# Performance work log

Measured on AMD Instinct MI355X. Metric: run time of the kernel, lower is better.

## Reference

```python
import jax, jax.numpy as jnp
import numpy as np

# Static config (matches init_kwargs / input_specs)
B, CIN, H, W = 8, 32, 96, 96
OC, KH, KW = 64, 3, 3
SH, SW = 1, 1
PAD = 1
P = 3                      # num_points
POS_MIN, POS_MAX = -1.0, 1.0
OH = (H + 2 * PAD - KH) // SH + 1   # 96
OW = (W + 2 * PAD - KW) // SW + 1   # 96
K = CIN * KH * KW                    # 288 reduction elements
S = OH * OW                          # 9216 output positions


def setup_inputs() -> dict:
    key = jax.random.key(0)
    k1, k2, k3 = jax.random.split(key, 3)
    x = jax.random.normal(k1, (B, CIN, H, W), dtype=jnp.float32)
    # positions: shared linspace over position_range, expanded per weight
    pos = jnp.broadcast_to(
        jnp.linspace(POS_MIN, POS_MAX, P, dtype=jnp.float32),
        (OC, CIN, KH, KW, P),
    )
    # values: linear ramp between two small random endpoints (start, end)
    start = 0.01 * jax.random.normal(k2, (OC, CIN, KH, KW), dtype=jnp.float32)
    end = 0.01 * jax.random.normal(k3, (OC, CIN, KH, KW), dtype=jnp.float32)
    w = jnp.linspace(0.0, 1.0, P, dtype=jnp.float32)
    values = start[..., None] * (1.0 - w) + end[..., None] * w
    return {"x": x, "positions": pos, "values": values}


def _unfold(x):
    """F.unfold equivalent: [B,CIN,H,W] -> [B, CIN*KH*KW, OH*OW], (c,kh,kw) order."""
    xp = jnp.pad(x, ((0, 0), (0, 0), (PAD, PAD), (PAD, PAD)))
    cols = [
        xp[:, :, kh : kh + OH * SH : SH, kw : kw + OW * SW : SW]
        for kh in range(KH)
        for kw in range(KW)
    ]
    patches = jnp.stack(cols, axis=2)  # [B, CIN, KH*KW, OH, OW]
    return patches.reshape(B, K, S)


def _piecewise_conv(x, positions, values):
    patches = _unfold(x)                      # [B, K, S]
    pos = positions.reshape(OC, K, P)
    val = values.reshape(OC, K, P)
    dp = pos[..., 1:] - pos[..., :-1]         # [OC, K, P-1]
    dv = val[..., 1:] - val[..., :-1]
    # slope 0 on degenerate intervals (pos_i == pos_{i+1} contributes val_i, as in kernel)
    slopes = jnp.where(dp > 0, dv / jnp.where(dp > 0, dp, 1.0), 0.0)

    # f(x) = val_0 + sum_i slope_i * (clip(x, pos_i, pos_{i+1}) - pos_i)
    # Exactly reproduces the kernel's piecewise-linear interp with left/right clamping
    # for sorted positions. Scan over the K reduction axis keeps the [B,OC,S]
    # broadcast intermediate small.
    xs = (
        patches.transpose(1, 0, 2),   # [K, B, S]
        pos.transpose(1, 0, 2),       # [K, OC, P]
        val.transpose(1, 0, 2),       # [K, OC, P]
        slopes.transpose(1, 0, 2),    # [K, OC, P-1]
    )

    def step(acc, inp):
        xk, pk, vk, sk = inp          # [B,S], [OC,P], [OC,P], [OC,P-1]
        f = jnp.broadcast_to(vk[None, :, 0, None], (B, OC, S))
        for i in range(P - 1):        # P is small & static
            t = jnp.clip(xk[:, None, :], pk[None, :, i, None], pk[None, :, i + 1, None])
            f = f + sk[None, :, i, None] * (t - pk[None, :, i, None])
        return acc + f, None

    out, _ = jax.lax.scan(step, jnp.zeros((B, OC, S), x.dtype), xs)
    return out.reshape(B, OC, OH, OW)


def reference(x, positions, values):
    return _piecewise_conv(x, positions, values)
```

## Files before the change

### kernel.cpp

```cpp
#include <hip/hip_runtime.h>


typedef _Float16 half8 __attribute__((ext_vector_type(8)));
typedef float floatx4 __attribute__((ext_vector_type(4)));
typedef float floatx16 __attribute__((ext_vector_type(16)));

#define CIN   32
#define OCN   64
#define HW    96
#define NCOL  98
#define NSTEP 36
#define WS_A_HALVES (NSTEP * 2 * 64 * 8)

__global__ __launch_bounds__(128) void prep_kernel(
    const float* __restrict__ pos, const float* __restrict__ val,
    _Float16* __restrict__ wsA, float* __restrict__ bias) {
  const int oc = blockIdx.x;
  const int t = threadIdx.x;
  __shared__ float csum[128];
  float cacc = 0.f;
  const float p0 = pos[0], p1 = pos[1], p2 = pos[2];
  const float r01 = (p1 > p0) ? 1.f / (p1 - p0) : 0.f;
  const float r12 = (p2 > p1) ? 1.f / (p2 - p1) : 0.f;
  if (t < 72) {
    const int s = t >> 1, khalf = t & 1;
    const int kk = s >> 1, s2 = s & 1;
    const int khkw = kk >> 1, c2 = kk & 1;
    half8 h;
#pragma unroll
    for (int j = 0; j < 8; ++j) {
      const int cin = s2 * 16 + khalf * 8 + j;
      const float* vb = val + ((size_t)(oc * CIN + cin) * 9 + khkw) * 3;
      const float V0 = vb[0], V1 = vb[1], V2 = vb[2];
      const float s0 = (V1 - V0) * r01, s1 = (V2 - V1) * r12;
      h[j] = (_Float16)(c2 ? s1 : s0);
      if (c2 == 0) cacc += V0 - s0 * p0 - s1 * p1;
    }
    *reinterpret_cast<half8*>(
        &wsA[(((size_t)s * 2 + (oc >> 5)) * 64 + khalf * 32 + (oc & 31)) * 8]) = h;
  }
  csum[t] = cacc;
  __syncthreads();
  for (int st = 64; st > 0; st >>= 1) {
    if (t < st) csum[t] += csum[t + st];
    __syncthreads();
  }
  if (t == 0) bias[oc] = csum[0];
}

__global__ __launch_bounds__(384, 5) void pwconv_kernel(
    const float* __restrict__ x, const float* __restrict__ pos,
    const _Float16* __restrict__ wsA, const float* __restrict__ bias,
    float* __restrict__ out) {
  const int blk = blockIdx.x;
  const int b  = blk & 7;
  const int oh = blk >> 3;
  const int tid = threadIdx.x;

  __shared__ alignas(16) _Float16 Bs[2 * 3 * 4 * NCOL * 8];

  const float p0 = pos[0], p1 = pos[1], p2 = pos[2];

  const int lane = tid & 63;
  const int wv   = tid >> 6;
  const int mG   = wv >> 1 == 0 ? 0 : (wv >= 3 ? 1 : 0);
  const int mG2  = wv / 3;
  const int nf   = wv % 3;
  const int l31  = lane & 31;
  const int q2   = lane >> 5;
  (void)mG;

  const _Float16* abase = wsA + (size_t)lane * 8;
  half8 a_cur = *reinterpret_cast<const half8*>(abase + (size_t)(0 * 2 + mG2) * 64 * 8);

  if (tid < 288) {
    const int cg  = tid % 24;
    const int t2  = tid / 24;
    const int chi = t2 & 3;
    const int row = t2 >> 2;
    const int xr = oh + row - 1;
    floatx4 v[8];
    if (xr >= 0 && xr < HW) {
      const float* src = x + (((size_t)b * CIN + chi * 8) * HW + xr) * HW + cg * 4;
#pragma unroll
      for (int j = 0; j < 8; ++j)
        v[j] = *reinterpret_cast<const floatx4*>(src + (size_t)j * HW * HW);
    } else {
#pragma unroll
      for (int j = 0; j < 8; ++j) v[j] = (floatx4){0.f, 0.f, 0.f, 0.f};
    }
#pragma unroll
    for (int c = 0; c < 4; ++c) {
      half8 a0, a1;
#pragma unroll
      for (int j = 0; j < 8; ++j) {
        const float tv = v[j][c];
        a0[j] = (_Float16)fminf(fmaxf(tv, p0), p1);
        a1[j] = (_Float16)fminf(fmaxf(tv, p1), p2);
      }
      const int col = 1 + cg * 4 + c;
      *reinterpret_cast<half8*>(&Bs[(((0 * 3 + row) * 4 + chi) * NCOL + col) * 8]) = a0;
      *reinterpret_cast<half8*>(&Bs[(((1 * 3 + row) * 4 + chi) * NCOL + col) * 8]) = a1;
    }
  } else if (tid < 312) {
    const int ht = tid - 288;
    const int col = (ht & 1) ? 97 : 0;
    const int chi = (ht >> 1) & 3;
    const int row = ht >> 3;
    const _Float16 h0 = (_Float16)fminf(fmaxf(0.f, p0), p1);
    const _Float16 h1 = (_Float16)fminf(fmaxf(0.f, p1), p2);
    half8 a0, a1;
#pragma unroll
    for (int j = 0; j < 8; ++j) { a0[j] = h0; a1[j] = h1; }
    *reinterpret_cast<half8*>(&Bs[(((0 * 3 + row) * 4 + chi) * NCOL + col) * 8]) = a0;
    *reinterpret_cast<half8*>(&Bs[(((1 * 3 + row) * 4 + chi) * NCOL + col) * 8]) = a1;
  }
  __syncthreads();

  floatx16 acc;
#pragma unroll
  for (int i = 0; i < 16; ++i) acc[i] = 0.f;

  const int lbase = q2 * NCOL + nf * 32 + l31;

#pragma unroll
  for (int s = 0; s < NSTEP; ++s) {
    half8 a_nxt;
    if (s + 1 < NSTEP)
      a_nxt = *reinterpret_cast<const half8*>(
          abase + (size_t)((s + 1) * 2 + mG2) * 64 * 8);
    const int khkw = s >> 2;
    const int c2   = (s >> 1) & 1;
    const int s2   = s & 1;
    const int kh   = khkw / 3;
    const int kw   = khkw - kh * 3;
    const half8 bf = *reinterpret_cast<const half8*>(
        &Bs[(((c2 * 3 + kh) * 4 + s2 * 2) * NCOL + kw + lbase) * 8]);
    acc = __builtin_amdgcn_mfma_f32_32x32x16_f16(a_cur, bf, acc, 0, 0, 0);
    a_cur = a_nxt;
  }

  const int ow = nf * 32 + l31;
#pragma unroll
  for (int g = 0; g < 4; ++g) {
    const int ocb = mG2 * 32 + g * 8 + q2 * 4;
    const floatx4 bv = *reinterpret_cast<const floatx4*>(&bias[ocb]);
#pragma unroll
    for (int i = 0; i < 4; ++i) {
      const size_t idx = (((size_t)b * OCN + ocb + i) * HW + oh) * HW + ow;
      out[idx] = acc[g * 4 + i] + bv[i];
    }
  }
}

extern "C" void kernel_launch(void* const* d_in, const int* in_sizes, int n_in,
                              void* d_out, int out_size, void* d_ws, size_t ws_size,
                              hipStream_t stream) {
  const float* x   = (const float*)d_in[0];
  const float* pos = (const float*)d_in[1];
  const float* val = (const float*)d_in[2];
  _Float16* wsA = (_Float16*)d_ws;
  float* bias = (float*)((char*)d_ws + WS_A_HALVES * 2);
  float* outp = (float*)d_out;

  prep_kernel<<<64, 128, 0, stream>>>(pos, val, wsA, bias);
  pwconv_kernel<<<8 * HW, 384, 0, stream>>>(x, pos, wsA, bias, outp);
}
```

Before: 79.61 us.

## Split K across waves with per-wave 3 N-tiles and LDS reduction

Changes the work split from 6 waves each owning one 32x32 output tile over the full K=36 steps to 4 waves, each owning an OC half and a K half (c2) across all three N tiles. Each A fragment is reused across three MFMAs, so global A loads per MFMA drop, and the two K halves are summed through LDS before the store. This adds an extra barrier and an LDS reduction, uses more accumulator registers, and lowers the thread count per block.

```diff
diff --git a/kernel.cpp b/kernel.cpp
--- a/kernel.cpp
+++ b/kernel.cpp
@@ -9,8 +9,7 @@
 #define OCN   64
 #define HW    96
 #define NCOL  98
-#define NSTEP 36
-#define WS_A_HALVES (NSTEP * 2 * 64 * 8)
+#define WS_A_HALVES (36 * 2 * 64 * 8)
 
 __global__ __launch_bounds__(128) void prep_kernel(
     const float* __restrict__ pos, const float* __restrict__ val,
@@ -48,7 +47,7 @@
   if (t == 0) bias[oc] = csum[0];
 }
 
-__global__ __launch_bounds__(384, 5) void pwconv_kernel(
+__global__ __launch_bounds__(256, 3) void pwconv_kernel(
     const float* __restrict__ x, const float* __restrict__ pos,
     const _Float16* __restrict__ wsA, const float* __restrict__ bias,
     float* __restrict__ out) {
@@ -63,92 +62,118 @@
 
   const int lane = tid & 63;
   const int wv   = tid >> 6;
-  const int mG   = wv >> 1 == 0 ? 0 : (wv >= 3 ? 1 : 0);
-  const int mG2  = wv / 3;
-  const int nf   = wv % 3;
+  const int mG2  = wv & 1;
+  const int c2   = wv >> 1;
   const int l31  = lane & 31;
   const int q2   = lane >> 5;
-  (void)mG;
 
   const _Float16* abase = wsA + (size_t)lane * 8;
-  half8 a_cur = *reinterpret_cast<const half8*>(abase + (size_t)(0 * 2 + mG2) * 64 * 8);
+#define AGIDX(s) ((size_t)((((s) >> 1) * 4 + c2 * 2 + ((s) & 1)) * 2 + mG2) * 64 * 8)
+  half8 a0 = *reinterpret_cast<const half8*>(abase + AGIDX(0));
+  half8 a1 = *reinterpret_cast<const half8*>(abase + AGIDX(1));
 
-  if (tid < 288) {
-    const int cg  = tid % 24;
-    const int t2  = tid / 24;
-    const int chi = t2 & 3;
-    const int row = t2 >> 2;
-    const int xr = oh + row - 1;
-    floatx4 v[8];
-    if (xr >= 0 && xr < HW) {
-      const float* src = x + (((size_t)b * CIN + chi * 8) * HW + xr) * HW + cg * 4;
+  for (int it = tid; it < 312; it += 256) {
+    if (it < 288) {
+      const int cg  = it % 24;
+      const int t2  = it / 24;
+      const int chi = t2 & 3;
+      const int row = t2 >> 2;
+      const int xr = oh + row - 1;
+      floatx4 v[8];
+      if (xr >= 0 && xr < HW) {
+        const float* src = x + (((size_t)b * CIN + chi * 8) * HW + xr) * HW + cg * 4;
 #pragma unroll
-      for (int j = 0; j < 8; ++j)
-        v[j] = *reinterpret_cast<const floatx4*>(src + (size_t)j * HW * HW);
+        for (int j = 0; j < 8; ++j)
+          v[j] = *reinterpret_cast<const floatx4*>(src + (size_t)j * HW * HW);
+      } else {
+#pragma unroll
+        for (int j = 0; j < 8; ++j) v[j] = (floatx4){0.f, 0.f, 0.f, 0.f};
+      }
+#pragma unroll
+      for (int c = 0; c < 4; ++c) {
+        half8 h0, h1;
+#pragma unroll
+        for (int j = 0; j < 8; ++j) {
+          const float tv = v[j][c];
+          h0[j] = (_Float16)fminf(fmaxf(tv, p0), p1);
+          h1[j] = (_Float16)fminf(fmaxf(tv, p1), p2);
+        }
+        const int col = 1 + cg * 4 + c;
+        *reinterpret_cast<half8*>(&Bs[(((0 * 3 + row) * 4 + chi) * NCOL + col) * 8]) = h0;
+        *reinterpret_cast<half8*>(&Bs[(((1 * 3 + row) * 4 + chi) * NCOL + col) * 8]) = h1;
+      }
     } else {
+      const int ht = it - 288;
+      const int col = (ht & 1) ? 97 : 0;
+      const int chi = (ht >> 1) & 3;
+      const int row = ht >> 3;
+      const _Float16 z0 = (_Float16)fminf(fmaxf(0.f, p0), p1);
+      const _Float16 z1 = (_Float16)fminf(fmaxf(0.f, p1), p2);
+      half8 h0, h1;
 #pragma unroll
-      for (int j = 0; j < 8; ++j) v[j] = (floatx4){0.f, 0.f, 0.f, 0.f};
+      for (int j = 0; j < 8; ++j) { h0[j] = z0; h1[j] = z1; }
+      *reinterpret_cast<half8*>(&Bs[(((0 * 3 + row) * 4 + chi) * NCOL + col) * 8]) = h0;
+      *reinterpret_cast<half8*>(&Bs[(((1 * 3 + row) * 4 + chi) * NCOL + col) * 8]) = h1;
     }
-#pragma unroll
-    for (int c = 0; c < 4; ++c) {
-      half8 a0, a1;
-#pragma unroll
-      for (int j = 0; j < 8; ++j) {
-        const float tv = v[j][c];
-        a0[j] = (_Float16)fminf(fmaxf(tv, p0), p1);
-        a1[j] = (_Float16)fminf(fmaxf(tv, p1), p2);
-      }
-      const int col = 1 + cg * 4 + c;
-      *reinterpret_cast<half8*>(&Bs[(((0 * 3 + row) * 4 + chi) * NCOL + col) * 8]) = a0;
-      *reinterpret_cast<half8*>(&Bs[(((1 * 3 + row) * 4 + chi) * NCOL + col) * 8]) = a1;
-    }
-  } else if (tid < 312) {
-    const int ht = tid - 288;
-    const int col = (ht & 1) ? 97 : 0;
-    const int chi = (ht >> 1) & 3;
-    const int row = ht >> 3;
-    const _Float16 h0 = (_Float16)fminf(fmaxf(0.f, p0), p1);
-    const _Float16 h1 = (_Float16)fminf(fmaxf(0.f, p1), p2);
-    half8 a0, a1;
-#pragma unroll
-    for (int j = 0; j < 8; ++j) { a0[j] = h0; a1[j] = h1; }
-    *reinterpret_cast<half8*>(&Bs[(((0 * 3 + row) * 4 + chi) * NCOL + col) * 8]) = a0;
-    *reinterpret_cast<half8*>(&Bs[(((1 * 3 + row) * 4 + chi) * NCOL + col) * 8]) = a1;
   }
   __syncthreads();
 
-  floatx16 acc;
+  floatx16 acc[3];
 #pragma unroll
-  for (int i = 0; i < 16; ++i) acc[i] = 0.f;
-
-  const int lbase = q2 * NCOL + nf * 32 + l31;
+  for (int nf = 0; nf < 3; ++nf)
+#pragma unroll
+    for (int i = 0; i < 16; ++i) acc[nf][i] = 0.f;
 
 #pragma unroll
-  for (int s = 0; s < NSTEP; ++s) {
-    half8 a_nxt;
-    if (s + 1 < NSTEP)
-      a_nxt = *reinterpret_cast<const half8*>(
-          abase + (size_t)((s + 1) * 2 + mG2) * 64 * 8);
-    const int khkw = s >> 2;
-    const int c2   = (s >> 1) & 1;
+  for (int s = 0; s < 18; ++s) {
+    half8 a2;
+    if (s + 2 < 18)
+      a2 = *reinterpret_cast<const half8*>(abase + AGIDX(s + 2));
+    const int khkw = s >> 1;
     const int s2   = s & 1;
     const int kh   = khkw / 3;
     const int kw   = khkw - kh * 3;
-    const half8 bf = *reinterpret_cast<const half8*>(
-        &Bs[(((c2 * 3 + kh) * 4 + s2 * 2) * NCOL + kw + lbase) * 8]);
-    acc = __builtin_amdgcn_mfma_f32_32x32x16_f16(a_cur, bf, acc, 0, 0, 0);
-    a_cur = a_nxt;
+    const int rbase = ((c2 * 3 + kh) * 4 + s2 * 2 + q2) * NCOL + kw + l31;
+#pragma unroll
+    for (int nf = 0; nf < 3; ++nf) {
+      const half8 bf = *reinterpret_cast<const half8*>(&Bs[(rbase + nf * 32) * 8]);
+      acc[nf] = __builtin_amdgcn_mfma_f32_32x32x16_f16(a0, bf, acc[nf], 0, 0, 0);
+    }
+    a0 = a1;
+    a1 = a2;
   }
+#undef AGIDX
 
-  const int ow = nf * 32 + l31;
+  __syncthreads();
+  float* red = reinterpret_cast<float*>(Bs);
+  if (c2 == 1) {
 #pragma unroll
-  for (int g = 0; g < 4; ++g) {
-    const int ocb = mG2 * 32 + g * 8 + q2 * 4;
-    const floatx4 bv = *reinterpret_cast<const floatx4*>(&bias[ocb]);
+    for (int nf = 0; nf < 3; ++nf)
 #pragma unroll
-    for (int i = 0; i < 4; ++i) {
-      const size_t idx = (((size_t)b * OCN + ocb + i) * HW + oh) * HW + ow;
-      out[idx] = acc[g * 4 + i] + bv[i];
+      for (int g = 0; g < 4; ++g) {
+        floatx4 v = {acc[nf][g * 4 + 0], acc[nf][g * 4 + 1],
+                     acc[nf][g * 4 + 2], acc[nf][g * 4 + 3]};
+        *reinterpret_cast<floatx4*>(
+            &red[(((mG2 * 3 + nf) * 4 + g) * 64 + lane) * 4]) = v;
+      }
+  }
+  __syncthreads();
+  if (c2 == 0) {
+#pragma unroll
+    for (int nf = 0; nf < 3; ++nf) {
+      const int ow = nf * 32 + l31;
+#pragma unroll
+      for (int g = 0; g < 4; ++g) {
+        const int ocb = mG2 * 32 + g * 8 + q2 * 4;
+        const floatx4 bv = *reinterpret_cast<const floatx4*>(&bias[ocb]);
+        const floatx4 r = *reinterpret_cast<const floatx4*>(
+            &red[(((mG2 * 3 + nf) * 4 + g) * 64 + lane) * 4]);
+#pragma unroll
+        for (int i = 0; i < 4; ++i) {
+          const size_t idx = (((size_t)b * OCN + ocb + i) * HW + oh) * HW + ow;
+          out[idx] = acc[nf][g * 4 + i] + r[i] + bv[i];
+        }
+      }
     }
   }
 }
@@ -164,5 +189,5 @@
   float* outp = (float*)d_out;
 
   prep_kernel<<<64, 128, 0, stream>>>(pos, val, wsA, bias);
-  pwconv_kernel<<<8 * HW, 384, 0, stream>>>(x, pos, wsA, bias, outp);
+  pwconv_kernel<<<8 * HW, 256, 0, stream>>>(x, pos, wsA, bias, outp);
 }
```

After: 80.14 us. No clear change (+0.7%).
